# Kernel tuning notes

Measured on AMD Instinct MI355X. Metric: run time of the kernel, lower is better.

The kernel has to match this reference:

```python
import jax, jax.numpy as jnp
import numpy as np

B, S, D, H = 4, 2048, 1024, 16
DK = D // H


def _rope(x):
    # x: [B, H, S, DK]; lucidrains rotary_embedding_torch default:
    # theta=10000, interleaved (rotate_half on (d/2, 2) pairs), freqs repeated pairwise.
    s, d = x.shape[-2], x.shape[-1]
    inv_freq = 1.0 / (10000.0 ** (jnp.arange(0, d, 2, dtype=jnp.float32) / d))  # [d/2]
    angles = jnp.arange(s, dtype=jnp.float32)[:, None] * inv_freq[None, :]      # [S, d/2]
    ang = jnp.repeat(angles, 2, axis=-1)                                        # [S, d] interleaved
    cos, sin = jnp.cos(ang), jnp.sin(ang)
    xp = x.reshape(*x.shape[:-1], d // 2, 2)
    rot = jnp.stack((-xp[..., 1], xp[..., 0]), axis=-1).reshape(x.shape)        # rotate_half
    return x * cos + rot * sin


def setup_inputs() -> dict:
    key = jax.random.key(0)
    ks = jax.random.split(key, 8)
    scale = 1.0 / np.sqrt(D)
    return {
        "q": jax.random.normal(ks[0], (B, S, D), dtype=jnp.float32),
        "k": jax.random.normal(ks[1], (B, S, D), dtype=jnp.float32),
        "v": jax.random.normal(ks[2], (B, S, D), dtype=jnp.float32),
        "mask": jax.random.randint(ks[3], (B, S), 0, 2, dtype=jnp.int32),
        "w_q": jax.random.normal(ks[4], (D, D), dtype=jnp.float32) * scale,
        "w_k": jax.random.normal(ks[5], (D, D), dtype=jnp.float32) * scale,
        "w_v": jax.random.normal(ks[6], (D, D), dtype=jnp.float32) * scale,
        "w_o": jax.random.normal(ks[7], (D, D), dtype=jnp.float32) * scale,
    }


def reference(q, k, v, mask, w_q, w_k, w_v, w_o):
    # Linear weights stored [out, in] as in torch; y = x @ W^T (bias=False).
    def split_heads(x):
        b, s, _ = x.shape
        return x.reshape(b, s, H, DK).transpose(0, 2, 1, 3)  # [B,H,S,DK]

    query = split_heads(q @ w_q.T)
    key_ = split_heads(k @ w_k.T)
    value = split_heads(v @ w_v.T)

    query = _rope(query)
    key_ = _rope(key_)

    scores = jnp.einsum("bhqd,bhkd->bhqk", query, key_) / np.sqrt(DK)
    scores = jnp.where(mask[:, None, None, :] == 0, -10000.0, scores)
    attn = jax.nn.softmax(scores, axis=-1)  # dropout is identity at eval
    x = jnp.einsum("bhqk,bhkd->bhqd", attn, value)
    x = x.transpose(0, 2, 1, 3).reshape(q.shape[0], -1, H * DK)
    return x @ w_o.T
```

## Files before the change

kernel.cpp:

```cpp
#include <hip/hip_runtime.h>
#include <hip/hip_bf16.h>
#include <math.h>


namespace {

constexpr int Bb = 4, Ss = 2048, Dd = 1024, Hh = 16, DKk = 64;
constexpr size_t NElem = (size_t)Bb * Hh * Ss * DKk;
constexpr size_t WElem = (size_t)Dd * Dd;

typedef __bf16 bf16;
typedef __attribute__((ext_vector_type(8))) __bf16 bf16x8;
typedef __attribute__((ext_vector_type(4))) float f32x4;

__device__ __forceinline__ bf16x8 pack8(float4 a, float4 b) {
  bf16x8 r;
  r[0] = (__bf16)a.x; r[1] = (__bf16)a.y; r[2] = (__bf16)a.z; r[3] = (__bf16)a.w;
  r[4] = (__bf16)b.x; r[5] = (__bf16)b.y; r[6] = (__bf16)b.z; r[7] = (__bf16)b.w;
  return r;
}

__device__ __forceinline__ void gl_lds16(const bf16* g, bf16* l) {
  __builtin_amdgcn_global_load_lds((const __attribute__((address_space(1))) void*)g,
                                   (__attribute__((address_space(3))) void*)l, 16, 0, 0);
}

__global__ __launch_bounds__(256) void cvt6(const float* __restrict__ q,
                                            const float* __restrict__ k,
                                            const float* __restrict__ v,
                                            const float* __restrict__ wq,
                                            const float* __restrict__ wk,
                                            const float* __restrict__ wv,
                                            const float* __restrict__ wo,
                                            bf16* __restrict__ xd, bf16* __restrict__ wd) {
  const int bid = blockIdx.x;
  const float* s; bf16* d; size_t idx;
  if (bid < 12288) {
    const int t = bid >> 12;
    s = (t == 0) ? q : (t == 1) ? k : v;
    d = xd + (size_t)t * NElem;
    idx = ((size_t)(bid & 4095) * 256 + threadIdx.x) * 8;
  } else {
    const int t = (bid - 12288) >> 9;
    s = (t == 0) ? wq : (t == 1) ? wk : (t == 2) ? wv : wo;
    d = wd + (size_t)t * WElem;
    idx = ((size_t)((bid - 12288) & 511) * 256 + threadIdx.x) * 8;
  }
  float4 f0 = *(const float4*)(s + idx), f1 = *(const float4*)(s + idx + 4);
  *(bf16x8*)(d + idx) = pack8(f0, f1);
}

__global__ __launch_bounds__(256) void cvt_pair(const float* __restrict__ x, bf16* __restrict__ xd,
                                                const float* __restrict__ ws, bf16* __restrict__ wd) {
  const int bid = blockIdx.x;
  const float* s; bf16* d; size_t idx;
  if (bid < 4096) { s = x; d = xd; idx = (size_t)bid * 256 + threadIdx.x; }
  else { s = ws; d = wd; idx = (size_t)(bid - 4096) * 256 + threadIdx.x; }
  idx *= 8;
  float4 f0 = *(const float4*)(s + idx), f1 = *(const float4*)(s + idx + 4);
  *(bf16x8*)(d + idx) = pack8(f0, f1);
}

__global__ __launch_bounds__(256) void cvt_w(const float* __restrict__ ws, bf16* __restrict__ wd) {
  size_t idx = ((size_t)blockIdx.x * 256 + threadIdx.x) * 8;
  float4 f0 = *(const float4*)(ws + idx), f1 = *(const float4*)(ws + idx + 4);
  *(bf16x8*)(wd + idx) = pack8(f0, f1);
}

template <int MODE>
__global__ __launch_bounds__(256, 4) void mha_gemm(const bf16* __restrict__ A,
                                                   const bf16* __restrict__ W,
                                                   void* __restrict__ dstv) {
  __shared__ __align__(16) bf16 As[2][128][32];
  __shared__ __align__(16) bf16 Bs[2][128][32];
  const int tid = threadIdx.x;
  const int z = (MODE == 3) ? blockIdx.z : 0;
  const int bm0 = blockIdx.x * 128, bn0 = blockIdx.y * 128;
  const int w = tid >> 6, lane = tid & 63, l16 = lane & 15, quad = lane >> 4;
  const int wm = (w >> 1) * 64, wn = (w & 1) * 64;
  const int lr = lane >> 2, lc = (lane & 3) * 8;

  const bf16* Ag = A + (size_t)z * NElem + (size_t)(bm0 + w * 32 + lr) * Dd + lc;
  const bf16* Wg = W + (size_t)z * WElem + (size_t)(bn0 + w * 32 + lr) * Dd + lc;

  f32x4 acc[4][4] = {};

  gl_lds16(Ag, &As[0][w * 32][0]);
  gl_lds16(Ag + 16 * Dd, &As[0][w * 32 + 16][0]);
  gl_lds16(Wg, &Bs[0][w * 32][0]);
  gl_lds16(Wg + 16 * Dd, &Bs[0][w * 32 + 16][0]);
  __syncthreads();

  for (int kt = 0; kt < 32; ++kt) {
    const int cur = kt & 1, nxt = cur ^ 1;
    if (kt < 31) {
      const int ko = (kt + 1) * 32;
      gl_lds16(Ag + ko, &As[nxt][w * 32][0]);
      gl_lds16(Ag + ko + 16 * Dd, &As[nxt][w * 32 + 16][0]);
      gl_lds16(Wg + ko, &Bs[nxt][w * 32][0]);
      gl_lds16(Wg + ko + 16 * Dd, &Bs[nxt][w * 32 + 16][0]);
    }
    bf16x8 af[4], bw[4];
#pragma unroll
    for (int i = 0; i < 4; ++i) af[i] = *(bf16x8*)&As[cur][wm + i * 16 + l16][quad * 8];
#pragma unroll
    for (int i = 0; i < 4; ++i) bw[i] = *(bf16x8*)&Bs[cur][wn + i * 16 + l16][quad * 8];
#pragma unroll
    for (int mt = 0; mt < 4; ++mt)
#pragma unroll
      for (int nt = 0; nt < 4; ++nt)
        acc[mt][nt] =
            __builtin_amdgcn_mfma_f32_16x16x32_bf16(af[mt], bw[nt], acc[mt][nt], 0, 0, 0);
    __syncthreads();
  }

  const bool do_rope = (MODE == 0) || (MODE == 3 && z < 2);
  const bool do_vt = (MODE == 1) || (MODE == 3 && z == 2);

  if constexpr (MODE == 2) {
    float* out = (float*)dstv;
#pragma unroll
    for (int mt = 0; mt < 4; ++mt)
#pragma unroll
      for (int nt = 0; nt < 4; ++nt) {
        const int gcol = bn0 + wn + nt * 16 + l16;
        const int grow0 = bm0 + wm + mt * 16 + quad * 4;
#pragma unroll
        for (int r = 0; r < 4; ++r) out[(size_t)(grow0 + r) * Dd + gcol] = acc[mt][nt][r];
      }
  } else {
    if (do_vt) {
      bf16* vt = (bf16*)dstv + (MODE == 3 ? 2 * NElem : 0);
#pragma unroll
      for (int mt = 0; mt < 4; ++mt)
#pragma unroll
        for (int nt = 0; nt < 4; ++nt) {
          const int gcol = bn0 + wn + nt * 16 + l16;
          const int h = gcol >> 6, dk = gcol & 63;
#pragma unroll
          for (int r = 0; r < 4; ++r) {
            const int grow = bm0 + wm + mt * 16 + quad * 4 + r;
            const int b = grow >> 11, s = grow & (Ss - 1);
            vt[((size_t)(b * Hh + h) * DKk + dk) * Ss + s] = (bf16)acc[mt][nt][r];
          }
        }
    } else if (do_rope) {
      bf16* qp = (bf16*)dstv + (MODE == 3 ? (size_t)z * NElem : 0);
#pragma unroll
      for (int mt = 0; mt < 4; ++mt)
#pragma unroll
        for (int nt = 0; nt < 4; ++nt) {
          const int gcol = bn0 + wn + nt * 16 + l16;
          const int h = gcol >> 6, dk = gcol & 63;
          const float invf = exp2f((float)(dk >> 1) * -0.4152410118609203f);
          const float sgn = (dk & 1) ? 1.0f : -1.0f;
#pragma unroll
          for (int r = 0; r < 4; ++r) {
            const int grow = bm0 + wm + mt * 16 + quad * 4 + r;
            const int b = grow >> 11, s = grow & (Ss - 1);
            const float v = acc[mt][nt][r];
            const float ov = __shfl_xor(v, 1);
            float sn, cs;
            __sincosf((float)s * invf, &sn, &cs);
            const float rot = v * cs + sgn * ov * sn;
            qp[((size_t)(b * Hh + h) * Ss + s) * DKk + dk] = (bf16)rot;
          }
        }
    }
  }
}

__global__ __launch_bounds__(256, 4) void mha_attn(const bf16* __restrict__ Qp,
                                                   const bf16* __restrict__ Kp,
                                                   const bf16* __restrict__ Vt,
                                                   const int* __restrict__ maskG,
                                                   bf16* __restrict__ Xo) {
  __shared__ __align__(16) bf16 Ks[2][64][64];
  __shared__ __align__(16) bf16 Vs[2][64][64];
  __shared__ __align__(16) bf16 Pbuf[4][1024];

  constexpr float c1 = 0.18033688011112042f;

  const int tid = threadIdx.x;
  const int bh = blockIdx.y, b = bh >> 4, h = bh & 15;
  const int q0 = blockIdx.x * 128;
  const int w = tid >> 6, lane = tid & 63, l16 = lane & 15, quad = lane >> 4;
  const int swz = l16 & 7;
  const size_t hbase = (size_t)bh * Ss * DKk;

  {
    bf16* Qst = &Ks[0][0][0];
    const int row = tid >> 1, hf = tid & 1;
    const bf16* src = Qp + hbase + (size_t)(q0 + row) * DKk + hf * 32;
#pragma unroll
    for (int cc = 0; cc < 4; ++cc)
      *(int4*)&Qst[(((hf * 4 + cc) * 128) + row) * 8] = *(const int4*)(src + cc * 8);
  }
  __syncthreads();
  bf16x8 qf[2][2];
  {
    const bf16* Qst = &Ks[0][0][0];
#pragma unroll
    for (int mt = 0; mt < 2; ++mt)
#pragma unroll
      for (int kk = 0; kk < 2; ++kk)
        qf[mt][kk] = *(bf16x8*)&Qst[(((kk * 4 + quad) * 128) + w * 32 + mt * 16 + l16) * 8];
  }
  __syncthreads();

  const int srow = lane >> 3, schunk = (lane & 7) ^ (srow & 7);
  const bf16* Kg = Kp + hbase + (size_t)(w * 16 + srow) * DKk + schunk * 8;
  const bf16* Vg = Vt + ((size_t)bh * DKk + w * 16 + srow) * Ss + schunk * 8;
  const int* Mg = maskG + b * Ss + l16;

  int mcur[4], mnext[4];
#pragma unroll
  for (int i = 0; i < 2; ++i) {
    gl_lds16(Kg + (size_t)i * 8 * DKk, &Ks[0][w * 16 + i * 8][0]);
    gl_lds16(Vg + i * 8 * Ss, &Vs[0][w * 16 + i * 8][0]);
  }
#pragma unroll
  for (int nt = 0; nt < 4; ++nt) mcur[nt] = Mg[nt * 16];
  __syncthreads();

  f32x4 o[2][4] = {};
  f32x4 lo[2] = {};
  bf16* Pb = &Pbuf[w][0];

  bf16x8 vones;
#pragma unroll
  for (int i = 0; i < 8; ++i) vones[i] = (__bf16)1.0f;

  for (int kt = 0; kt < 32; ++kt) {
    const int cur = kt & 1, nxt = cur ^ 1;
    if (kt < 31) {
      const size_t k0n = (size_t)(kt + 1) * 64;
#pragma unroll
      for (int i = 0; i < 2; ++i) {
        gl_lds16(Kg + k0n * DKk + (size_t)i * 8 * DKk, &Ks[nxt][w * 16 + i * 8][0]);
        gl_lds16(Vg + k0n + i * 8 * Ss, &Vs[nxt][w * 16 + i * 8][0]);
      }
#pragma unroll
      for (int nt = 0; nt < 4; ++nt) mnext[nt] = Mg[k0n + nt * 16];
    }

    f32x4 sc[2][4];
#pragma unroll
    for (int nt = 0; nt < 4; ++nt) {
      const float bv = (mcur[nt] != 0) ? -96.0f : -1e9f;
#pragma unroll
      for (int r = 0; r < 4; ++r) { sc[0][nt][r] = bv; sc[1][nt][r] = bv; }
    }
#pragma unroll
    for (int kk = 0; kk < 2; ++kk)
#pragma unroll
      for (int nt = 0; nt < 4; ++nt) {
        bf16x8 kf = *(bf16x8*)&Ks[cur][nt * 16 + l16][((kk * 4 + quad) ^ swz) * 8];
        sc[0][nt] = __builtin_amdgcn_mfma_f32_16x16x32_bf16(qf[0][kk], kf, sc[0][nt], 0, 0, 0);
        sc[1][nt] = __builtin_amdgcn_mfma_f32_16x16x32_bf16(qf[1][kk], kf, sc[1][nt], 0, 0, 0);
      }

    bf16x8 pf0[2], pf1[2];
#pragma unroll
    for (int nt = 0; nt < 4; ++nt) {
      const int c = nt * 2 + (l16 >> 3);
      const int jj = l16 & 7;
#pragma unroll
      for (int r = 0; r < 4; ++r)
        Pb[(c * 16 + quad * 4 + r) * 8 + jj] = (bf16)exp2f(sc[0][nt][r] * c1);
    }
#pragma unroll
    for (int kk = 0; kk < 2; ++kk)
      pf0[kk] = *(bf16x8*)(Pb + ((kk * 4 + quad) * 16 + l16) * 8);
#pragma unroll
    for (int nt = 0; nt < 4; ++nt) {
      const int c = nt * 2 + (l16 >> 3);
      const int jj = l16 & 7;
#pragma unroll
      for (int r = 0; r < 4; ++r)
        Pb[(c * 16 + quad * 4 + r) * 8 + jj] = (bf16)exp2f(sc[1][nt][r] * c1);
    }
#pragma unroll
    for (int kk = 0; kk < 2; ++kk)
      pf1[kk] = *(bf16x8*)(Pb + ((kk * 4 + quad) * 16 + l16) * 8);

#pragma unroll
    for (int kk = 0; kk < 2; ++kk) {
      lo[0] = __builtin_amdgcn_mfma_f32_16x16x32_bf16(pf0[kk], vones, lo[0], 0, 0, 0);
      lo[1] = __builtin_amdgcn_mfma_f32_16x16x32_bf16(pf1[kk], vones, lo[1], 0, 0, 0);
#pragma unroll
      for (int nt = 0; nt < 4; ++nt) {
        bf16x8 vf = *(bf16x8*)&Vs[cur][nt * 16 + l16][((kk * 4 + quad) ^ swz) * 8];
        o[0][nt] = __builtin_amdgcn_mfma_f32_16x16x32_bf16(pf0[kk], vf, o[0][nt], 0, 0, 0);
        o[1][nt] = __builtin_amdgcn_mfma_f32_16x16x32_bf16(pf1[kk], vf, o[1][nt], 0, 0, 0);
      }
    }
    __syncthreads();
#pragma unroll
    for (int nt = 0; nt < 4; ++nt) mcur[nt] = mnext[nt];
  }

#pragma unroll
  for (int mt = 0; mt < 2; ++mt)
#pragma unroll
    for (int nt = 0; nt < 4; ++nt)
#pragma unroll
      for (int r = 0; r < 4; ++r) {
        const int srw = q0 + w * 32 + mt * 16 + quad * 4 + r;
        const int dk = nt * 16 + l16;
        Xo[(size_t)(b * Ss + srw) * Dd + h * DKk + dk] = (bf16)(o[mt][nt][r] / lo[mt][r]);
      }
}

}

extern "C" void kernel_launch(void* const* d_in, const int* in_sizes, int n_in,
                              void* d_out, int out_size, void* d_ws, size_t ws_size,
                              hipStream_t stream) {
  (void)in_sizes; (void)n_in; (void)out_size;
  const float* q = (const float*)d_in[0];
  const float* k = (const float*)d_in[1];
  const float* v = (const float*)d_in[2];
  const int* mask = (const int*)d_in[3];
  const float* w_q = (const float*)d_in[4];
  const float* w_k = (const float*)d_in[5];
  const float* w_v = (const float*)d_in[6];
  const float* w_o = (const float*)d_in[7];
  float* out = (float*)d_out;

  dim3 blk(256);
  const size_t fused_bytes = (6 * NElem + 4 * WElem) * sizeof(bf16);

  if (ws_size >= fused_bytes) {
    bf16* Ab = (bf16*)d_ws;
    bf16* Wb = Ab + 3 * NElem;
    bf16* Db = Wb + 4 * WElem;
    bf16* Qp = Db;
    bf16* Kp = Db + NElem;
    bf16* Vt = Db + 2 * NElem;
    bf16* Xo = Ab;

    cvt6<<<14336, blk, 0, stream>>>(q, k, v, w_q, w_k, w_v, w_o, Ab, Wb);
    mha_gemm<3><<<dim3(64, 8, 3), blk, 0, stream>>>(Ab, Wb, (void*)Db);
    mha_attn<<<dim3(16, 64), blk, 0, stream>>>(Qp, Kp, Vt, mask, Xo);
    mha_gemm<2><<<dim3(64, 8), blk, 0, stream>>>(Xo, Wb + 3 * WElem, (void*)out);
  } else {
    bf16* buf0 = (bf16*)d_ws;
    bf16* wbuf = buf0 + NElem;
    bf16* Qp = wbuf + WElem;
    bf16* Kp = Qp + NElem;
    bf16* Vt = Kp + NElem;

    dim3 g(64, 8);
    cvt_pair<<<4608, blk, 0, stream>>>(q, buf0, w_q, wbuf);
    mha_gemm<0><<<g, blk, 0, stream>>>(buf0, wbuf, (void*)Qp);
    cvt_pair<<<4608, blk, 0, stream>>>(k, buf0, w_k, wbuf);
    mha_gemm<0><<<g, blk, 0, stream>>>(buf0, wbuf, (void*)Kp);
    cvt_pair<<<4608, blk, 0, stream>>>(v, buf0, w_v, wbuf);
    mha_gemm<1><<<g, blk, 0, stream>>>(buf0, wbuf, (void*)Vt);
    mha_attn<<<dim3(16, 64), blk, 0, stream>>>(Qp, Kp, Vt, mask, buf0);
    cvt_w<<<512, blk, 0, stream>>>(w_o, wbuf);
    mha_gemm<2><<<g, blk, 0, stream>>>(buf0, wbuf, (void*)out);
  }
}
```

Before: 364.2 us.

## Triple-buffer GEMM LDS tiles with partial vmcnt waits for deeper prefetch

Turns the double-buffered K loop of the projection GEMM into a three-stage pipeline. Loads are issued two tiles ahead, and the barrier now waits only on the older group of global-to-LDS loads through an explicit s_waitcnt vmcnt(4), replacing __syncthreads. The goal is to hide more global load latency behind the MFMA work. In exchange LDS use rises from 32KB to 48KB per block, and launch bounds drop from 4 to 3 blocks per CU, which may reduce occupancy.

```diff
diff --git a/kernel.cpp b/kernel.cpp
--- a/kernel.cpp
+++ b/kernel.cpp
@@ -68,11 +68,11 @@
 }
 
 template <int MODE>
-__global__ __launch_bounds__(256, 4) void mha_gemm(const bf16* __restrict__ A,
+__global__ __launch_bounds__(256, 3) void mha_gemm(const bf16* __restrict__ A,
                                                    const bf16* __restrict__ W,
                                                    void* __restrict__ dstv) {
-  __shared__ __align__(16) bf16 As[2][128][32];
-  __shared__ __align__(16) bf16 Bs[2][128][32];
+  __shared__ __align__(16) bf16 As[3][128][32];
+  __shared__ __align__(16) bf16 Bs[3][128][32];
   const int tid = threadIdx.x;
   const int z = (MODE == 3) ? blockIdx.z : 0;
   const int bm0 = blockIdx.x * 128, bn0 = blockIdx.y * 128;
@@ -85,21 +85,25 @@
 
   f32x4 acc[4][4] = {};
 
-  gl_lds16(Ag, &As[0][w * 32][0]);
-  gl_lds16(Ag + 16 * Dd, &As[0][w * 32 + 16][0]);
-  gl_lds16(Wg, &Bs[0][w * 32][0]);
-  gl_lds16(Wg + 16 * Dd, &Bs[0][w * 32 + 16][0]);
-  __syncthreads();
-
+#define STAGE(buf, kt)                                      \
+  do {                                                      \
+    const int ko_ = (kt) * 32;                              \
+    gl_lds16(Ag + ko_, &As[(buf)][w * 32][0]);              \
+    gl_lds16(Ag + ko_ + 16 * Dd, &As[(buf)][w * 32 + 16][0]); \
+    gl_lds16(Wg + ko_, &Bs[(buf)][w * 32][0]);              \
+    gl_lds16(Wg + ko_ + 16 * Dd, &Bs[(buf)][w * 32 + 16][0]); \
+  } while (0)
+
+  STAGE(0, 0);
+  STAGE(1, 1);
+  asm volatile("s_waitcnt vmcnt(4)" ::: "memory");
+  __builtin_amdgcn_s_barrier();
+  __builtin_amdgcn_sched_barrier(0);
+
+  int cur = 0, stb = 2;
   for (int kt = 0; kt < 32; ++kt) {
-    const int cur = kt & 1, nxt = cur ^ 1;
-    if (kt < 31) {
-      const int ko = (kt + 1) * 32;
-      gl_lds16(Ag + ko, &As[nxt][w * 32][0]);
-      gl_lds16(Ag + ko + 16 * Dd, &As[nxt][w * 32 + 16][0]);
-      gl_lds16(Wg + ko, &Bs[nxt][w * 32][0]);
-      gl_lds16(Wg + ko + 16 * Dd, &Bs[nxt][w * 32 + 16][0]);
-    }
+    if (kt < 30) STAGE(stb, kt + 2);
+
     bf16x8 af[4], bw[4];
 #pragma unroll
     for (int i = 0; i < 4; ++i) af[i] = *(bf16x8*)&As[cur][wm + i * 16 + l16][quad * 8];
@@ -111,8 +115,20 @@
       for (int nt = 0; nt < 4; ++nt)
         acc[mt][nt] =
             __builtin_amdgcn_mfma_f32_16x16x32_bf16(af[mt], bw[nt], acc[mt][nt], 0, 0, 0);
-    __syncthreads();
-  }
+
+    __builtin_amdgcn_sched_barrier(0);
+    if (kt < 30) {
+      asm volatile("s_waitcnt vmcnt(4)" ::: "memory");
+    } else {
+      asm volatile("s_waitcnt vmcnt(0)" ::: "memory");
+    }
+    __builtin_amdgcn_s_barrier();
+    __builtin_amdgcn_sched_barrier(0);
+
+    cur = (cur == 2) ? 0 : cur + 1;
+    stb = (stb == 2) ? 0 : stb + 1;
+  }
+#undef STAGE
 
   const bool do_rope = (MODE == 0) || (MODE == 3 && z < 2);
   const bool do_vt = (MODE == 1) || (MODE == 3 && z == 2);
```

Measured after the change: 364.0 us. No clear change (-0.1%).
